# Optimization experiments

Hardware: AMD Instinct MI355X
Metric: run time of the kernel (lower is better)

## Reference

```python
import jax, jax.numpy as jnp
import numpy as np

B, M, K = 8, 2048, 64          # clouds, points per cloud, max neighbors
C_IN, C_OUT, R = 64, 64, 0.2   # channels, radius
BN_EPS = 1e-5                  # BatchNorm eval: running_mean=0, running_var=1


def _bn(y, g, b):
    # eval-mode BatchNorm1d with running stats (0, 1)
    return g * y * (1.0 / jnp.sqrt(1.0 + BN_EPS)) + b


def _lin_init(key, fan_in, shape):
    s = 1.0 / np.sqrt(fan_in)
    return jax.random.uniform(key, shape, jnp.float32, -s, s)


def setup_inputs() -> dict:
    key = jax.random.key(0)
    ks = jax.random.split(key, 16)
    N = B * M
    pos = jax.random.uniform(ks[0], (N, 3), jnp.float32)
    x = jax.random.normal(ks[1], (N, C_IN), jnp.float32)
    nrm = jax.random.normal(ks[2], (N, 3), jnp.float32)
    normal = nrm / jnp.linalg.norm(nrm, axis=-1, keepdims=True)
    batch = jnp.repeat(jnp.arange(B, dtype=jnp.int32), M)
    return {
        "x": x, "pos": pos, "normal": normal, "batch": batch,
        # PointTransformerConv linear layers (value / key / query)
        "lin_w": _lin_init(ks[3], C_IN, (C_IN, C_OUT)),
        "lin_b": _lin_init(ks[4], C_IN, (C_OUT,)),
        "lin_src_w": _lin_init(ks[5], C_IN, (C_IN, C_OUT)),
        "lin_src_b": _lin_init(ks[6], C_IN, (C_OUT,)),
        "lin_dst_w": _lin_init(ks[7], C_IN, (C_IN, C_OUT)),
        "lin_dst_b": _lin_init(ks[8], C_IN, (C_OUT,)),
        # pos_nn = MLP([6, C_OUT]): Linear -> BN -> ReLU (Dropout off in eval)
        "pos_w": _lin_init(ks[9], 6, (6, C_OUT)),
        "pos_b": _lin_init(ks[10], 6, (C_OUT,)),
        "pos_g": jnp.ones((C_OUT,), jnp.float32),
        "pos_bt": jnp.zeros((C_OUT,), jnp.float32),
        # attn_nn = MLP([C_OUT, C_OUT])
        "attn_w": _lin_init(ks[11], C_OUT, (C_OUT, C_OUT)),
        "attn_b": _lin_init(ks[12], C_OUT, (C_OUT,)),
        "attn_g": jnp.ones((C_OUT,), jnp.float32),
        "attn_bt": jnp.zeros((C_OUT,), jnp.float32),
    }


def _forward(x, pos, normal, lin_w, lin_b, lin_src_w, lin_src_b,
             lin_dst_w, lin_dst_b, pos_w, pos_b, pos_g, pos_bt,
             attn_w, attn_b, attn_g, attn_bt):
    xb = x.reshape(B, M, C_IN)
    pb = pos.reshape(B, M, 3)
    nb = normal.reshape(B, M, 3)

    # radius(pos, pos, r, batch, batch, max_num_neighbors=K):
    # per-cloud pairwise sq-distances -> K nearest, masked to d <= r.
    d2 = jnp.sum((pb[:, :, None, :] - pb[:, None, :, :]) ** 2, axis=-1)  # [B,M,M]
    neg_d2, idx = jax.lax.top_k(-d2, K)                                   # [B,M,K]
    mask = (-neg_d2) <= R * R                                             # self always valid

    gather = jax.vmap(lambda a, i: a[i])  # per-cloud gather: [M,C],[M,K] -> [M,K,C]

    v = xb @ lin_w + lin_b          # value   [B,M,C]
    kf = xb @ lin_src_w + lin_src_b # key     [B,M,C]
    q = xb @ lin_dst_w + lin_dst_b  # query   [B,M,C]

    vj = gather(v, idx)             # [B,M,K,C]
    kj = gather(kf, idx)
    pj = gather(pb, idx)            # [B,M,K,3]
    nj = gather(nb, idx)

    rel = jnp.concatenate([pb[:, :, None, :] - pj,
                           nb[:, :, None, :] - nj], axis=-1)  # [B,M,K,6]
    delta = jax.nn.relu(_bn(rel @ pos_w + pos_b, pos_g, pos_bt))  # [B,M,K,C]

    alpha = jax.nn.relu(_bn((q[:, :, None, :] - kj + delta) @ attn_w + attn_b,
                            attn_g, attn_bt))                     # [B,M,K,C]
    alpha = jnp.where(mask[..., None], alpha, -jnp.inf)
    w = jax.nn.softmax(alpha, axis=2)                              # softmax over neighbors

    out = jnp.sum(w * (vj + delta), axis=2)                        # [B,M,C]
    return out.reshape(B * M, C_OUT)


def reference(x, pos, normal, batch, lin_w, lin_b, lin_src_w, lin_src_b,
              lin_dst_w, lin_dst_b, pos_w, pos_b, pos_g, pos_bt,
              attn_w, attn_b, attn_g, attn_bt):
    del batch  # batch ids are block-contiguous: encoded by the [B,M] reshape
    return _forward(x, pos, normal, lin_w, lin_b, lin_src_w, lin_src_b,
                    lin_dst_w, lin_dst_b, pos_w, pos_b, pos_g, pos_bt,
                    attn_w, attn_b, attn_g, attn_bt)
```

## Files before the change

kernel.cpp:

```cpp
#include <hip/hip_runtime.h>
#include <math.h>

#define BB 8
#define MM 2048
#define KK 64
#define CC 64
#define NTOT (BB*MM)
#define R2 0.04f
#define CAP 256

typedef _Float16 h8 __attribute__((ext_vector_type(8)));
typedef _Float16 h4 __attribute__((ext_vector_type(4)));
typedef float f32x4 __attribute__((ext_vector_type(4)));

__device__ __forceinline__ int swz(int row, int col) {
  return (row << 6) + ((((col >> 3) ^ (row & 7)) << 3) | (col & 7));
}

__device__ __forceinline__ unsigned long long shfl_xor_u64(unsigned long long x, int off) {
  int lo = __shfl_xor((int)(unsigned)(x & 0xFFFFFFFFull), off, 64);
  int hi = __shfl_xor((int)(unsigned)(x >> 32), off, 64);
  return (((unsigned long long)(unsigned)hi) << 32) | (unsigned)lo;
}

__device__ __forceinline__ unsigned long long wave_min_u64(unsigned long long x) {
#pragma unroll
  for (int off = 32; off; off >>= 1) {
    unsigned long long o = shfl_xor_u64(x, off);
    x = (o < x) ? o : x;
  }
  return x;
}

__device__ __forceinline__ unsigned long long wave_max_u64(unsigned long long x) {
#pragma unroll
  for (int off = 32; off; off >>= 1) {
    unsigned long long o = shfl_xor_u64(x, off);
    x = (o > x) ? o : x;
  }
  return x;
}

__global__ __launch_bounds__(256) void prep_w(
    const float* __restrict__ attn_w, const float* __restrict__ pos_w,
    const float* __restrict__ lin_w, const float* __restrict__ lsw, const float* __restrict__ ldw,
    const float* __restrict__ pos_b, const float* __restrict__ pos_g, const float* __restrict__ pos_bt,
    const float* __restrict__ attn_b, const float* __restrict__ attn_g, const float* __restrict__ attn_bt,
    unsigned short* __restrict__ w_img, unsigned short* __restrict__ pw_img,
    unsigned short* __restrict__ pj_img, float* __restrict__ bnc) {
  const int idx = blockIdx.x * 256 + threadIdx.x;
  const float bninv = 1.0f / sqrtf(1.0f + 1e-5f);
  if (idx < 4096) {
    const int d = idx >> 6, cc = idx & 63;
    const int sp = swz(cc, d);
    w_img[sp] = __builtin_bit_cast(unsigned short, (_Float16)attn_w[idx]);
    const float v0 = lin_w[idx];
    const _Float16 h0 = (_Float16)v0;
    pj_img[sp] = __builtin_bit_cast(unsigned short, h0);
    pj_img[4096 + sp] = __builtin_bit_cast(unsigned short, (_Float16)(v0 - (float)h0));
    const float v1 = lsw[idx];
    const _Float16 h1 = (_Float16)v1;
    pj_img[8192 + sp] = __builtin_bit_cast(unsigned short, h1);
    pj_img[12288 + sp] = __builtin_bit_cast(unsigned short, (_Float16)(v1 - (float)h1));
    const float v2 = ldw[idx];
    const _Float16 h2 = (_Float16)v2;
    pj_img[16384 + sp] = __builtin_bit_cast(unsigned short, h2);
    pj_img[20480 + sp] = __builtin_bit_cast(unsigned short, (_Float16)(v2 - (float)h2));
  }
  if (idx < 64 * 24) {
    const int col = idx / 24, k = idx - col * 24;
    const float v = (k < 6) ? pos_w[k * 64 + col] : 0.f;
    pw_img[idx] = __builtin_bit_cast(unsigned short, (_Float16)v);
  }
  if (idx < 64) {
    const float pA = pos_g[idx] * bninv;
    bnc[idx] = pA;
    bnc[64 + idx] = pA * pos_b[idx] + pos_bt[idx];
    const float aA = attn_g[idx] * bninv;
    bnc[128 + idx] = aA;
    bnc[192 + idx] = aA * attn_b[idx] + attn_bt[idx];
  }
}

__global__ __launch_bounds__(256, 2) void proj_mfma(
    const float* __restrict__ x, const unsigned short* __restrict__ pj_img,
    const float* __restrict__ b0, const float* __restrict__ b1, const float* __restrict__ b2,
    float* __restrict__ o0, float* __restrict__ o1, float* __restrict__ o2) {
  __shared__ __align__(16) unsigned short s_xh[4096];
  __shared__ __align__(16) unsigned short s_xl[4096];
  __shared__ __align__(16) unsigned short s_w6[6 * 4096];
  const int tid = threadIdx.x;
  const int r0 = blockIdx.x << 6;
  for (int i = tid; i < 3072; i += 256)
    ((uint4*)s_w6)[i] = ((const uint4*)pj_img)[i];
  {
    const int row = tid >> 2, seg = tid & 3;
    const float* xr = x + (((size_t)(r0 + row)) << 6) + (seg << 4);
    float xb[16];
#pragma unroll
    for (int q = 0; q < 4; ++q) *(float4*)&xb[q * 4] = ((const float4*)xr)[q];
    h8 c0h, c1h, c0l, c1l;
#pragma unroll
    for (int e = 0; e < 8; ++e) {
      const _Float16 h0 = (_Float16)xb[e];
      c0h[e] = h0; c0l[e] = (_Float16)(xb[e] - (float)h0);
      const _Float16 h1 = (_Float16)xb[e + 8];
      c1h[e] = h1; c1l[e] = (_Float16)(xb[e + 8] - (float)h1);
    }
    const int base = row << 6;
    const int oi0 = base + ((((seg << 1) | 0) ^ (row & 7)) << 3);
    const int oi1 = base + ((((seg << 1) | 1) ^ (row & 7)) << 3);
    *(h8*)&s_xh[oi0] = c0h; *(h8*)&s_xh[oi1] = c1h;
    *(h8*)&s_xl[oi0] = c0l; *(h8*)&s_xl[oi1] = c1l;
  }
  __syncthreads();
  const int wv = tid >> 6, lane = tid & 63, lrow = lane >> 4, lcol = lane & 15;
  const int col = (wv << 4) + lcol;
  f32x4 acc[3][4];
#pragma unroll
  for (int o = 0; o < 3; ++o)
#pragma unroll
    for (int mt = 0; mt < 4; ++mt) acc[o][mt] = (f32x4){0.f, 0.f, 0.f, 0.f};
#pragma unroll
  for (int ks = 0; ks < 2; ++ks) {
    const int kc = lrow + (ks << 2);
    const int boff = (col << 6) + ((kc ^ (col & 7)) << 3);
    const h8 bh0 = *(const h8*)&s_w6[boff];
    const h8 bl0 = *(const h8*)&s_w6[4096 + boff];
    const h8 bh1 = *(const h8*)&s_w6[8192 + boff];
    const h8 bl1 = *(const h8*)&s_w6[12288 + boff];
    const h8 bh2 = *(const h8*)&s_w6[16384 + boff];
    const h8 bl2 = *(const h8*)&s_w6[20480 + boff];
#pragma unroll
    for (int mt = 0; mt < 4; ++mt) {
      const int m = (mt << 4) + lcol;
      const int aoff = (m << 6) + ((kc ^ (m & 7)) << 3);
      const h8 ah = *(const h8*)&s_xh[aoff];
      const h8 al = *(const h8*)&s_xl[aoff];
      acc[0][mt] = __builtin_amdgcn_mfma_f32_16x16x32_f16(ah, bh0, acc[0][mt], 0, 0, 0);
      acc[0][mt] = __builtin_amdgcn_mfma_f32_16x16x32_f16(al, bh0, acc[0][mt], 0, 0, 0);
      acc[0][mt] = __builtin_amdgcn_mfma_f32_16x16x32_f16(ah, bl0, acc[0][mt], 0, 0, 0);
      acc[1][mt] = __builtin_amdgcn_mfma_f32_16x16x32_f16(ah, bh1, acc[1][mt], 0, 0, 0);
      acc[1][mt] = __builtin_amdgcn_mfma_f32_16x16x32_f16(al, bh1, acc[1][mt], 0, 0, 0);
      acc[1][mt] = __builtin_amdgcn_mfma_f32_16x16x32_f16(ah, bl1, acc[1][mt], 0, 0, 0);
      acc[2][mt] = __builtin_amdgcn_mfma_f32_16x16x32_f16(ah, bh2, acc[2][mt], 0, 0, 0);
      acc[2][mt] = __builtin_amdgcn_mfma_f32_16x16x32_f16(al, bh2, acc[2][mt], 0, 0, 0);
      acc[2][mt] = __builtin_amdgcn_mfma_f32_16x16x32_f16(ah, bl2, acc[2][mt], 0, 0, 0);
    }
  }
  const float bb0 = b0[col], bb1 = b1[col], bb2 = b2[col];
#pragma unroll
  for (int mt = 0; mt < 4; ++mt)
#pragma unroll
    for (int r = 0; r < 4; ++r) {
      const size_t gi = (((size_t)(r0 + (mt << 4) + (lrow << 2) + r)) << 6) + col;
      o0[gi] = acc[0][mt][r] + bb0;
      o1[gi] = acc[1][mt][r] + bb1;
      o2[gi] = acc[2][mt][r] + bb2;
    }
}

__global__ __launch_bounds__(256) void knn_kernel(const float* __restrict__ pos,
                                                  unsigned* __restrict__ nbr) {
  __shared__ float spos[MM * 3];
  __shared__ unsigned long long slist[4][CAP];
  const int bidx = blockIdx.x;
  const int b = bidx >> 9;
  const int qblk = bidx & 511;
  const int tid = threadIdx.x;
  const float* pc = pos + (size_t)b * MM * 3;
  for (int i = tid; i < MM * 3 / 4; i += 256)
    ((float4*)spos)[i] = ((const float4*)pc)[i];
  __syncthreads();
  const int wv = tid >> 6, lane = tid & 63;
  const int q = (qblk << 2) + wv;
  const float qx = spos[q * 3 + 0], qy = spos[q * 3 + 1], qz = spos[q * 3 + 2];
  unsigned bits[32];
  unsigned cnt = 0;
#pragma unroll
  for (int i = 0; i < 32; ++i) {
    const int j = lane + (i << 6);
    const float dx = qx - spos[j * 3 + 0];
    const float dy = qy - spos[j * 3 + 1];
    const float dz = qz - spos[j * 3 + 2];
    const float d2 = __fadd_rn(__fadd_rn(__fmul_rn(dx, dx), __fmul_rn(dy, dy)), __fmul_rn(dz, dz));
    const unsigned bt = __float_as_uint(d2);
    bits[i] = bt;
    const bool val = (d2 <= R2);
    const unsigned long long mb = __ballot(val);
    if (val) {
      const unsigned off = cnt + (unsigned)__popcll(mb & ((1ull << lane) - 1ull));
      if (off < CAP) slist[wv][off] = (((unsigned long long)bt) << 32) | (unsigned)j;
    }
    cnt += (unsigned)__popcll(mb);
  }
  __syncthreads();
  unsigned outv;
  if (cnt <= 64u) {
    if (lane < (int)cnt) outv = ((unsigned)slist[wv][lane]) | 0x80000000u;
    else                 outv = 0u;
  } else if (cnt <= (unsigned)CAP) {
    unsigned long long s0, s1, s2, s3, t;
    s0 = (lane       < (int)cnt) ? slist[wv][lane      ] : ~0ull;
    s1 = (lane + 64  < (int)cnt) ? slist[wv][lane + 64 ] : ~0ull;
    s2 = (lane + 128 < (int)cnt) ? slist[wv][lane + 128] : ~0ull;
    s3 = (lane + 192 < (int)cnt) ? slist[wv][lane + 192] : ~0ull;
    if (s1 < s0) { t = s0; s0 = s1; s1 = t; }
    if (s3 < s2) { t = s2; s2 = s3; s3 = t; }
    if (s2 < s0) { t = s0; s0 = s2; s2 = t; }
    if (s3 < s1) { t = s1; s1 = s3; s3 = t; }
    if (s2 < s1) { t = s1; s1 = s2; s2 = t; }
    if (cnt <= 128u) {
      const int pops = (int)cnt - 64;
      int rl = (cnt > (unsigned)lane) ? (int)((cnt - (unsigned)lane + 63u) >> 6) : 0;
      if (rl > 4) rl = 4;
      int ti = rl - 1;
      for (int p = 0; p < pops; ++p) {
        const unsigned long long mx =
            (ti == 3) ? s3 : (ti == 2) ? s2 : (ti == 1) ? s1 : (ti == 0) ? s0 : 0ull;
        const unsigned long long g = wave_max_u64(mx);
        if (ti >= 0 && mx == g) ti--;
      }
      const int c = ti + 1;
      const unsigned long long b0 = __ballot(c & 1);
      const unsigned long long b1 = __ballot(c & 2);
      const unsigned long long b2 = __ballot(c & 4);
      const unsigned long long lm = (1ull << lane) - 1ull;
      const int pre = __popcll(b0 & lm) + 2 * __popcll(b1 & lm) + 4 * __popcll(b2 & lm);
      if (c > 0) slist[wv][pre + 0] = s0;
      if (c > 1) slist[wv][pre + 1] = s1;
      if (c > 2) slist[wv][pre + 2] = s2;
      if (c > 3) slist[wv][pre + 3] = s3;
      __asm volatile("s_waitcnt lgkmcnt(0)" ::: "memory");
      outv = ((unsigned)slist[wv][lane]) | 0x80000000u;
    } else {
      unsigned long long my = 0;
      for (int it = 0; it < 64; ++it) {
        const unsigned long long gg = wave_min_u64(s0);
        if (lane == it) my = gg;
        if (s0 == gg) { s0 = s1; s1 = s2; s2 = s3; s3 = ~0ull; }
      }
      outv = ((unsigned)my) | 0x80000000u;
    }
  } else {
    unsigned long long cur = ~0ull;
#pragma unroll
    for (int i = 0; i < 32; ++i) {
      const unsigned long long k = (((unsigned long long)bits[i]) << 32) | (unsigned)(lane + (i << 6));
      cur = (k < cur) ? k : cur;
    }
    unsigned long long my = 0;
    for (int it = 0; it < 64; ++it) {
      const unsigned long long gg = wave_min_u64(cur);
      if (lane == it) my = gg;
      if (cur == gg) {
        cur = ~0ull;
#pragma unroll
        for (int i = 0; i < 32; ++i) {
          const unsigned long long k = (((unsigned long long)bits[i]) << 32) | (unsigned)(lane + (i << 6));
          if (k > gg && k < cur) cur = k;
        }
      }
    }
    const float d2s = __uint_as_float((unsigned)(my >> 32));
    outv = ((unsigned)my) | ((d2s <= R2) ? 0x80000000u : 0u);
  }
  nbr[((size_t)(b * MM + q)) * 64 + lane] = outv;
}

__global__ __launch_bounds__(256, 4) void ptc_kernel(
    const float* __restrict__ pos, const float* __restrict__ nrm,
    const float* __restrict__ vv, const float* __restrict__ kf, const float* __restrict__ qq,
    const unsigned* __restrict__ nbr,
    const unsigned short* __restrict__ w_img, const unsigned short* __restrict__ pw_img,
    const float* __restrict__ bnc,
    float* __restrict__ out) {
  __shared__ __align__(16) unsigned short s_w[4096];
  __shared__ __align__(16) unsigned short s_kt[4096];
  __shared__ __align__(16) unsigned short s_vv[4096];
  __shared__ __align__(16) unsigned short s_pw[64 * 24];
  __shared__ __align__(16) unsigned short s_relh[64 * 24];
  __shared__ unsigned s_sel[64];
  const int qi = blockIdx.x;
  const int b = qi >> 11;
  const int tid = threadIdx.x;
  const int wv = tid >> 6, lane = tid & 63;
  const int lrow = lane >> 4, lcol = lane & 15;
  const int col = (wv << 4) + lcol;

  if (tid < 64) s_sel[tid] = nbr[(size_t)qi * 64 + tid];
  {
    const uint4* wi = (const uint4*)w_img;
    uint4* sw = (uint4*)s_w;
    sw[tid] = wi[tid];
    sw[tid + 256] = wi[tid + 256];
    if (tid < 192) ((uint4*)s_pw)[tid] = ((const uint4*)pw_img)[tid];
  }
  __syncthreads();

  {
    const int row = tid >> 2, seg = tid & 3;
    const int j = (int)(s_sel[row] & 0x7FFFFFFFu);
    const size_t rb = (((size_t)((b << 11) + j)) << 6) + (seg << 4);
    const float* kr = kf + rb;
    const float* vr = vv + rb;
    float kb[16], vb[16];
#pragma unroll
    for (int q = 0; q < 4; ++q) {
      *(float4*)&kb[q * 4] = ((const float4*)kr)[q];
      *(float4*)&vb[q * 4] = ((const float4*)vr)[q];
    }
    h8 kc0, kc1, vc0, vc1;
#pragma unroll
    for (int e = 0; e < 8; ++e) {
      kc0[e] = (_Float16)kb[e]; kc1[e] = (_Float16)kb[e + 8];
      vc0[e] = (_Float16)vb[e]; vc1[e] = (_Float16)vb[e + 8];
    }
    const int base = row << 6;
    const int oi0 = base + ((((seg << 1) | 0) ^ (row & 7)) << 3);
    const int oi1 = base + ((((seg << 1) | 1) ^ (row & 7)) << 3);
    *(h8*)&s_kt[oi0] = kc0; *(h8*)&s_kt[oi1] = kc1;
    *(h8*)&s_vv[oi0] = vc0; *(h8*)&s_vv[oi1] = vc1;
  }
  if (tid < 64) {
    const int j = (int)(s_sel[tid] & 0x7FFFFFFFu);
    const int jg = (b << 11) + j;
    h8 hv;
    hv[0] = (_Float16)(pos[(size_t)qi * 3 + 0] - pos[(size_t)jg * 3 + 0]);
    hv[1] = (_Float16)(pos[(size_t)qi * 3 + 1] - pos[(size_t)jg * 3 + 1]);
    hv[2] = (_Float16)(pos[(size_t)qi * 3 + 2] - pos[(size_t)jg * 3 + 2]);
    hv[3] = (_Float16)(nrm[(size_t)qi * 3 + 0] - nrm[(size_t)jg * 3 + 0]);
    hv[4] = (_Float16)(nrm[(size_t)qi * 3 + 1] - nrm[(size_t)jg * 3 + 1]);
    hv[5] = (_Float16)(nrm[(size_t)qi * 3 + 2] - nrm[(size_t)jg * 3 + 2]);
    hv[6] = (_Float16)0.f; hv[7] = (_Float16)0.f;
    *(h8*)&s_relh[tid * 24] = hv;
    h8 zz = (h8)(_Float16)0.f;
    *(h8*)&s_relh[tid * 24 + 8] = zz;
  }
  __syncthreads();

  f32x4 dacc[4];
  {
    const h4 bpw = *(const h4*)&s_pw[col * 24 + (lrow << 2)];
#pragma unroll
    for (int mt = 0; mt < 4; ++mt) {
      const h4 ar = *(const h4*)&s_relh[((mt << 4) + lcol) * 24 + (lrow << 2)];
      dacc[mt] = __builtin_amdgcn_mfma_f32_16x16x16f16(ar, bpw, (f32x4){0.f, 0.f, 0.f, 0.f}, 0, 0, 0);
    }
  }

  const float pA = bnc[col], pB = bnc[64 + col];
  const float aA = bnc[128 + col], aB = bnc[192 + col];
  const float qvc = qq[(size_t)qi * 64 + col];
  float def[16];
#pragma unroll
  for (int mt = 0; mt < 4; ++mt) {
#pragma unroll
    for (int r = 0; r < 4; ++r) {
      const int i = (mt << 2) + r;
      const int n = (mt << 4) + (lrow << 2) + r;
      const int hw = swz(n, col);
      const float kv = (float)*(const _Float16*)&s_kt[hw];
      const float de = fmaxf(fmaf(pA, dacc[mt][r], pB), 0.f);
      def[i] = de;
      const float t = qvc - kv + de;
      *(_Float16*)&s_kt[hw] = (_Float16)t;
    }
  }
  __syncthreads();

  f32x4 acc[4];
#pragma unroll
  for (int mt = 0; mt < 4; ++mt) acc[mt] = (f32x4){0.f, 0.f, 0.f, 0.f};
#pragma unroll
  for (int ks = 0; ks < 2; ++ks) {
    const int kc = lrow + (ks << 2);
    const h8 bh = *(const h8*)&s_w[(col << 6) + ((kc ^ (col & 7)) << 3)];
#pragma unroll
    for (int mt = 0; mt < 4; ++mt) {
      const int m = (mt << 4) + lcol;
      const h8 ah = *(const h8*)&s_kt[(m << 6) + ((kc ^ (m & 7)) << 3)];
      acc[mt] = __builtin_amdgcn_mfma_f32_16x16x32_f16(ah, bh, acc[mt], 0, 0, 0);
    }
  }

  float a[16];
  float pm = -INFINITY;
#pragma unroll
  for (int mt = 0; mt < 4; ++mt) {
    const uint4 s4 = *(const uint4*)&s_sel[(mt << 4) + (lrow << 2)];
    const unsigned sv[4] = {s4.x, s4.y, s4.z, s4.w};
#pragma unroll
    for (int r = 0; r < 4; ++r) {
      const int i = (mt << 2) + r;
      const float al = fmaxf(fmaf(aA, acc[mt][r], aB), 0.f);
      const float av = (sv[r] >> 31) ? al : -INFINITY;
      a[i] = av;
      pm = fmaxf(pm, av);
    }
  }
  pm = fmaxf(pm, __shfl_xor(pm, 16, 64));
  pm = fmaxf(pm, __shfl_xor(pm, 32, 64));
  float ps = 0.f;
#pragma unroll
  for (int i = 0; i < 16; ++i) {
    const float e = __expf(a[i] - pm);
    a[i] = e;
    ps += e;
  }
  ps += __shfl_xor(ps, 16, 64);
  ps += __shfl_xor(ps, 32, 64);

  float o = 0.f;
#pragma unroll
  for (int mt = 0; mt < 4; ++mt) {
#pragma unroll
    for (int r = 0; r < 4; ++r) {
      const int i = (mt << 2) + r;
      const int n = (mt << 4) + (lrow << 2) + r;
      const float vj = (float)*(const _Float16*)&s_vv[swz(n, col)];
      o = fmaf(a[i], vj + def[i], o);
    }
  }
  o += __shfl_xor(o, 16, 64);
  o += __shfl_xor(o, 32, 64);
  if (lrow == 0) out[(size_t)qi * 64 + col] = o * (1.0f / ps);
}

extern "C" void kernel_launch(void* const* d_in, const int* in_sizes, int n_in,
                              void* d_out, int out_size, void* d_ws, size_t ws_size,
                              hipStream_t stream) {
  const float* x      = (const float*)d_in[0];
  const float* pos    = (const float*)d_in[1];
  const float* nrm    = (const float*)d_in[2];
  const float* lin_w  = (const float*)d_in[4];
  const float* lin_b  = (const float*)d_in[5];
  const float* lsw    = (const float*)d_in[6];
  const float* lsb    = (const float*)d_in[7];
  const float* ldw    = (const float*)d_in[8];
  const float* ldb    = (const float*)d_in[9];
  const float* pos_w  = (const float*)d_in[10];
  const float* pos_b  = (const float*)d_in[11];
  const float* pos_g  = (const float*)d_in[12];
  const float* pos_bt = (const float*)d_in[13];
  const float* attn_w = (const float*)d_in[14];
  const float* attn_b = (const float*)d_in[15];
  const float* attn_g = (const float*)d_in[16];
  const float* attn_bt= (const float*)d_in[17];
  float* out = (float*)d_out;

  float* wsf = (float*)d_ws;
  float* v   = wsf;
  float* kf  = wsf + (size_t)NTOT * 64;
  float* qv  = wsf + (size_t)2 * NTOT * 64;
  unsigned* nbr = (unsigned*)(wsf + (size_t)3 * NTOT * 64);
  unsigned short* w_img  = (unsigned short*)(wsf + (size_t)4 * NTOT * 64);
  unsigned short* pw_img = w_img + 4096;
  unsigned short* pj_img = pw_img + 1536;
  float* bnc = (float*)(pj_img + 24576);

  prep_w<<<16, 256, 0, stream>>>(attn_w, pos_w, lin_w, lsw, ldw,
                                 pos_b, pos_g, pos_bt, attn_b, attn_g, attn_bt,
                                 w_img, pw_img, pj_img, bnc);
  proj_mfma<<<NTOT / 64, 256, 0, stream>>>(
      x, pj_img, lin_b, lsb, ldb, v, kf, qv);
  knn_kernel<<<BB * (MM / 4), 256, 0, stream>>>(pos, nbr);
  ptc_kernel<<<NTOT, 256, 0, stream>>>(
      pos, nrm, v, kf, qv, nbr, w_img, pw_img, bnc, out);
}
```

Before: 131.4 us.

## Fold attention weight into key/query projections and drop per-query K/V LDS staging

Uses linearity of the attention linear layer: precomputes lin_src_w@attn_w and lin_dst_w@attn_w (plus biases) so the projection kernel emits key and query values already multiplied by attn_w. Inside the per-query kernel, only the positional delta goes through the MFMA. The projected key and query terms are added per column afterwards. Neighbor key and value features are read directly from global memory into registers instead of being staged, converted and swizzled in LDS. This cuts LDS traffic and a barrier stage, but adds uncoalesced per-column gathers and a small extra weight-fusion kernel, and slightly changes rounding.

```diff
diff --git a/kernel.cpp b/kernel.cpp
--- a/kernel.cpp
+++ b/kernel.cpp
@@ -3,8 +3,6 @@
 
 #define BB 8
 #define MM 2048
-#define KK 64
-#define CC 64
 #define NTOT (BB*MM)
 #define R2 0.04f
 #define CAP 256
@@ -22,7 +20,6 @@
   int hi = __shfl_xor((int)(unsigned)(x >> 32), off, 64);
   return (((unsigned long long)(unsigned)hi) << 32) | (unsigned)lo;
 }
-
 __device__ __forceinline__ unsigned long long wave_min_u64(unsigned long long x) {
 #pragma unroll
   for (int off = 32; off; off >>= 1) {
@@ -31,7 +28,6 @@
   }
   return x;
 }
-
 __device__ __forceinline__ unsigned long long wave_max_u64(unsigned long long x) {
 #pragma unroll
   for (int off = 32; off; off >>= 1) {
@@ -41,11 +37,41 @@
   return x;
 }
 
+__global__ __launch_bounds__(256) void fuse_w(
+    const float* __restrict__ lsw, const float* __restrict__ ldw, const float* __restrict__ attn_w,
+    const float* __restrict__ lsb, const float* __restrict__ ldb,
+    float* __restrict__ wka, float* __restrict__ wqa,
+    float* __restrict__ bka, float* __restrict__ bqa, float* __restrict__ zvec) {
+  __shared__ float sA[4096], sB[4096];
+  const int tid = threadIdx.x;
+  const float* src = blockIdx.x ? ldw : lsw;
+  const float* sbv = blockIdx.x ? ldb : lsb;
+  float* dst = blockIdx.x ? wqa : wka;
+  float* dbv = blockIdx.x ? bqa : bka;
+  for (int i = tid; i < 4096; i += 256) { sA[i] = src[i]; sB[i] = attn_w[i]; }
+  __syncthreads();
+  const int c = tid & 63, ig = tid >> 6;
+#pragma unroll
+  for (int r = 0; r < 16; ++r) {
+    const int i = ig * 16 + r;
+    float acc = 0.f;
+    for (int d = 0; d < 64; ++d) acc = fmaf(sA[i * 64 + d], sB[d * 64 + c], acc);
+    dst[i * 64 + c] = acc;
+  }
+  if (tid < 64) {
+    float acc = 0.f;
+    for (int d = 0; d < 64; ++d) acc = fmaf(sbv[d], sB[d * 64 + tid], acc);
+    dbv[tid] = acc;
+    if (blockIdx.x == 0) zvec[tid] = 0.f;
+  }
+}
+
 __global__ __launch_bounds__(256) void prep_w(
     const float* __restrict__ attn_w, const float* __restrict__ pos_w,
-    const float* __restrict__ lin_w, const float* __restrict__ lsw, const float* __restrict__ ldw,
+    const float* __restrict__ lin_w, const float* __restrict__ wka, const float* __restrict__ wqa,
     const float* __restrict__ pos_b, const float* __restrict__ pos_g, const float* __restrict__ pos_bt,
     const float* __restrict__ attn_b, const float* __restrict__ attn_g, const float* __restrict__ attn_bt,
+    const float* __restrict__ bka, const float* __restrict__ bqa,
     unsigned short* __restrict__ w_img, unsigned short* __restrict__ pw_img,
     unsigned short* __restrict__ pj_img, float* __restrict__ bnc) {
   const int idx = blockIdx.x * 256 + threadIdx.x;
@@ -58,11 +84,11 @@
     const _Float16 h0 = (_Float16)v0;
     pj_img[sp] = __builtin_bit_cast(unsigned short, h0);
     pj_img[4096 + sp] = __builtin_bit_cast(unsigned short, (_Float16)(v0 - (float)h0));
-    const float v1 = lsw[idx];
+    const float v1 = wka[idx];
     const _Float16 h1 = (_Float16)v1;
     pj_img[8192 + sp] = __builtin_bit_cast(unsigned short, h1);
     pj_img[12288 + sp] = __builtin_bit_cast(unsigned short, (_Float16)(v1 - (float)h1));
-    const float v2 = ldw[idx];
+    const float v2 = wqa[idx];
     const _Float16 h2 = (_Float16)v2;
     pj_img[16384 + sp] = __builtin_bit_cast(unsigned short, h2);
     pj_img[20480 + sp] = __builtin_bit_cast(unsigned short, (_Float16)(v2 - (float)h2));
@@ -78,7 +104,7 @@
     bnc[64 + idx] = pA * pos_b[idx] + pos_bt[idx];
     const float aA = attn_g[idx] * bninv;
     bnc[128 + idx] = aA;
-    bnc[192 + idx] = aA * attn_b[idx] + attn_bt[idx];
+    bnc[192 + idx] = aA * (attn_b[idx] + bqa[idx] - bka[idx]) + attn_bt[idx];
   }
 }
 
@@ -270,17 +296,15 @@
 
 __global__ __launch_bounds__(256, 4) void ptc_kernel(
     const float* __restrict__ pos, const float* __restrict__ nrm,
-    const float* __restrict__ vv, const float* __restrict__ kf, const float* __restrict__ qq,
+    const float* __restrict__ vv, const float* __restrict__ kwr, const float* __restrict__ qwr,
     const unsigned* __restrict__ nbr,
     const unsigned short* __restrict__ w_img, const unsigned short* __restrict__ pw_img,
     const float* __restrict__ bnc,
     float* __restrict__ out) {
   __shared__ __align__(16) unsigned short s_w[4096];
-  __shared__ __align__(16) unsigned short s_kt[4096];
-  __shared__ __align__(16) unsigned short s_vv[4096];
+  __shared__ __align__(16) unsigned short s_t[4096];
   __shared__ __align__(16) unsigned short s_pw[64 * 24];
   __shared__ __align__(16) unsigned short s_relh[64 * 24];
-  __shared__ unsigned s_sel[64];
   const int qi = blockIdx.x;
   const int b = qi >> 11;
   const int tid = threadIdx.x;
@@ -288,43 +312,35 @@
   const int lrow = lane >> 4, lcol = lane & 15;
   const int col = (wv << 4) + lcol;
 
-  if (tid < 64) s_sel[tid] = nbr[(size_t)qi * 64 + tid];
-  {
-    const uint4* wi = (const uint4*)w_img;
-    uint4* sw = (uint4*)s_w;
-    sw[tid] = wi[tid];
-    sw[tid + 256] = wi[tid + 256];
-    if (tid < 192) ((uint4*)s_pw)[tid] = ((const uint4*)pw_img)[tid];
-  }
-  __syncthreads();
-
-  {
-    const int row = tid >> 2, seg = tid & 3;
-    const int j = (int)(s_sel[row] & 0x7FFFFFFFu);
-    const size_t rb = (((size_t)((b << 11) + j)) << 6) + (seg << 4);
-    const float* kr = kf + rb;
-    const float* vr = vv + rb;
-    float kb[16], vb[16];
-#pragma unroll
-    for (int q = 0; q < 4; ++q) {
-      *(float4*)&kb[q * 4] = ((const float4*)kr)[q];
-      *(float4*)&vb[q * 4] = ((const float4*)vr)[q];
-    }
-    h8 kc0, kc1, vc0, vc1;
-#pragma unroll
-    for (int e = 0; e < 8; ++e) {
-      kc0[e] = (_Float16)kb[e]; kc1[e] = (_Float16)kb[e + 8];
-      vc0[e] = (_Float16)vb[e]; vc1[e] = (_Float16)vb[e + 8];
-    }
-    const int base = row << 6;
-    const int oi0 = base + ((((seg << 1) | 0) ^ (row & 7)) << 3);
-    const int oi1 = base + ((((seg << 1) | 1) ^ (row & 7)) << 3);
-    *(h8*)&s_kt[oi0] = kc0; *(h8*)&s_kt[oi1] = kc1;
-    *(h8*)&s_vv[oi0] = vc0; *(h8*)&s_vv[oi1] = vc1;
-  }
+  uint4 sraw[4];
+#pragma unroll
+  for (int mt = 0; mt < 4; ++mt)
+    sraw[mt] = *(const uint4*)&nbr[(size_t)qi * 64 + (mt << 4) + (lrow << 2)];
+
+  float kwv[16], vvv[16];
+  unsigned mbits = 0;
+#pragma unroll
+  for (int mt = 0; mt < 4; ++mt) {
+    const unsigned sv[4] = {sraw[mt].x, sraw[mt].y, sraw[mt].z, sraw[mt].w};
+#pragma unroll
+    for (int r = 0; r < 4; ++r) {
+      const int i = (mt << 2) + r;
+      const unsigned s = sv[r];
+      mbits |= ((s >> 31) & 1u) << i;
+      const size_t jg = ((size_t)(b << 11) + (size_t)(s & 0x7FFFFFFFu));
+      kwv[i] = kwr[(jg << 6) + col];
+      vvv[i] = vv[(jg << 6) + col];
+    }
+  }
+  const float qwc = qwr[(size_t)qi * 64 + col];
+
+  ((uint4*)s_w)[tid] = ((const uint4*)w_img)[tid];
+  ((uint4*)s_w)[tid + 256] = ((const uint4*)w_img)[tid + 256];
+  if (tid < 192) ((uint4*)s_pw)[tid] = ((const uint4*)pw_img)[tid];
+
   if (tid < 64) {
-    const int j = (int)(s_sel[tid] & 0x7FFFFFFFu);
-    const int jg = (b << 11) + j;
+    const unsigned s = nbr[(size_t)qi * 64 + tid];
+    const int jg = (b << 11) + (int)(s & 0x7FFFFFFFu);
     h8 hv;
     hv[0] = (_Float16)(pos[(size_t)qi * 3 + 0] - pos[(size_t)jg * 3 + 0]);
     hv[1] = (_Float16)(pos[(size_t)qi * 3 + 1] - pos[(size_t)jg * 3 + 1]);
@@ -350,8 +366,8 @@
   }
 
   const float pA = bnc[col], pB = bnc[64 + col];
-  const float aA = bnc[128 + col], aB = bnc[192 + col];
-  const float qvc = qq[(size_t)qi * 64 + col];
+  const float aA = bnc[128 + col];
+  const float aBq = fmaf(aA, qwc, bnc[192 + col]);
   float def[16];
 #pragma unroll
   for (int mt = 0; mt < 4; ++mt) {
@@ -359,12 +375,9 @@
     for (int r = 0; r < 4; ++r) {
       const int i = (mt << 2) + r;
       const int n = (mt << 4) + (lrow << 2) + r;
-      const int hw = swz(n, col);
-      const float kv = (float)*(const _Float16*)&s_kt[hw];
       const float de = fmaxf(fmaf(pA, dacc[mt][r], pB), 0.f);
       def[i] = de;
-      const float t = qvc - kv + de;
-      *(_Float16*)&s_kt[hw] = (_Float16)t;
+      *(_Float16*)&s_t[swz(n, col)] = (_Float16)de;
     }
   }
   __syncthreads();
@@ -379,7 +392,7 @@
 #pragma unroll
     for (int mt = 0; mt < 4; ++mt) {
       const int m = (mt << 4) + lcol;
-      const h8 ah = *(const h8*)&s_kt[(m << 6) + ((kc ^ (m & 7)) << 3)];
+      const h8 ah = *(const h8*)&s_t[(m << 6) + ((kc ^ (m & 7)) << 3)];
       acc[mt] = __builtin_amdgcn_mfma_f32_16x16x32_f16(ah, bh, acc[mt], 0, 0, 0);
     }
   }
@@ -388,13 +401,11 @@
   float pm = -INFINITY;
 #pragma unroll
   for (int mt = 0; mt < 4; ++mt) {
-    const uint4 s4 = *(const uint4*)&s_sel[(mt << 4) + (lrow << 2)];
-    const unsigned sv[4] = {s4.x, s4.y, s4.z, s4.w};
 #pragma unroll
     for (int r = 0; r < 4; ++r) {
       const int i = (mt << 2) + r;
-      const float al = fmaxf(fmaf(aA, acc[mt][r], aB), 0.f);
-      const float av = (sv[r] >> 31) ? al : -INFINITY;
+      const float al = fmaxf(fmaf(aA, acc[mt][r] - kwv[i], aBq), 0.f);
+      const float av = ((mbits >> i) & 1u) ? al : -INFINITY;
       a[i] = av;
       pm = fmaxf(pm, av);
     }
@@ -413,15 +424,7 @@
 
   float o = 0.f;
 #pragma unroll
-  for (int mt = 0; mt < 4; ++mt) {
-#pragma unroll
-    for (int r = 0; r < 4; ++r) {
-      const int i = (mt << 2) + r;
-      const int n = (mt << 4) + (lrow << 2) + r;
-      const float vj = (float)*(const _Float16*)&s_vv[swz(n, col)];
-      o = fmaf(a[i], vj + def[i], o);
-    }
-  }
+  for (int i = 0; i < 16; ++i) o = fmaf(a[i], vvv[i] + def[i], o);
   o += __shfl_xor(o, 16, 64);
   o += __shfl_xor(o, 32, 64);
   if (lrow == 0) out[(size_t)qi * 64 + col] = o * (1.0f / ps);
@@ -450,21 +453,27 @@
   float* out = (float*)d_out;
 
   float* wsf = (float*)d_ws;
-  float* v   = wsf;
-  float* kf  = wsf + (size_t)NTOT * 64;
-  float* qv  = wsf + (size_t)2 * NTOT * 64;
+  float* v    = wsf;
+  float* kwr  = wsf + (size_t)NTOT * 64;
+  float* qwrp = wsf + (size_t)2 * NTOT * 64;
   unsigned* nbr = (unsigned*)(wsf + (size_t)3 * NTOT * 64);
   unsigned short* w_img  = (unsigned short*)(wsf + (size_t)4 * NTOT * 64);
   unsigned short* pw_img = w_img + 4096;
   unsigned short* pj_img = pw_img + 1536;
-  float* bnc = (float*)(pj_img + 24576);
-
-  prep_w<<<16, 256, 0, stream>>>(attn_w, pos_w, lin_w, lsw, ldw,
+  float* bnc  = (float*)(pj_img + 24576);
+  float* wka  = bnc + 256;
+  float* wqa  = wka + 4096;
+  float* bka  = wqa + 4096;
+  float* bqa  = bka + 64;
+  float* zvec = bqa + 64;
+
+  fuse_w<<<2, 256, 0, stream>>>(lsw, ldw, attn_w, lsb, ldb, wka, wqa, bka, bqa, zvec);
+  prep_w<<<16, 256, 0, stream>>>(attn_w, pos_w, lin_w, wka, wqa,
                                  pos_b, pos_g, pos_bt, attn_b, attn_g, attn_bt,
-                                 w_img, pw_img, pj_img, bnc);
+                                 bka, bqa, w_img, pw_img, pj_img, bnc);
   proj_mfma<<<NTOT / 64, 256, 0, stream>>>(
-      x, pj_img, lin_b, lsb, ldb, v, kf, qv);
+      x, pj_img, lin_b, zvec, zvec, v, kwr, qwrp);
   knn_kernel<<<BB * (MM / 4), 256, 0, stream>>>(pos, nbr);
   ptc_kernel<<<NTOT, 256, 0, stream>>>(
-      pos, nrm, v, kf, qv, nbr, w_img, pw_img, bnc, out);
-}
+      pos, nrm, v, kwr, qwrp, nbr, w_img, pw_img, bnc, out);
+}
```

Result: slower. 158.6 us (+20.7%).
